# Optimization experiments

Hardware: AMD Instinct MI355X
Metric: run time of the kernel (lower is better)

## Reference

```python
import jax, jax.numpy as jnp
import numpy as np

DIM = 2048
N_HEADS = 32
HEAD_DIM = DIM // N_HEADS
D_FF = 4 * DIM
EPS = 1e-5


def layernorm(x, g, b):
    mu = jnp.mean(x, axis=-1, keepdims=True)
    var = jnp.mean(jnp.square(x - mu), axis=-1, keepdims=True)
    return (x - mu) * jax.lax.rsqrt(var + EPS) * g + b


def setup_inputs() -> dict:
    key = jax.random.key(0)
    ks = jax.random.split(key, 12)
    s = 0.02
    # Linear weights stored as [in, out] (y = x @ W + b), equivalent math to torch's x @ W.T
    return {
        "x": jax.random.normal(ks[0], (2, 2048, DIM), jnp.float32),
        "w_qkv": jax.random.normal(ks[1], (DIM, 3 * DIM), jnp.float32) * s,
        "b_qkv": jnp.zeros((3 * DIM,), jnp.float32),
        "w_o": jax.random.normal(ks[2], (DIM, DIM), jnp.float32) * s,
        "b_o": jnp.zeros((DIM,), jnp.float32),
        "g1": jnp.ones((DIM,), jnp.float32),
        "beta1": jnp.zeros((DIM,), jnp.float32),
        "w1": jax.random.normal(ks[3], (DIM, D_FF), jnp.float32) * s,
        "b1": jnp.zeros((D_FF,), jnp.float32),
        "w2": jax.random.normal(ks[4], (D_FF, DIM), jnp.float32) * s,
        "b2": jnp.zeros((DIM,), jnp.float32),
        "g2": jnp.ones((DIM,), jnp.float32),
        "beta2": jnp.zeros((DIM,), jnp.float32),
    }


def reference(x, w_qkv, b_qkv, w_o, b_o, g1, beta1, w1, b1, w2, b2, g2, beta2):
    B, T, _ = x.shape
    residual = x
    h = layernorm(x, g1, beta1)
    qkv = h @ w_qkv + b_qkv                      # [B,T,3*DIM]
    qkv = qkv.reshape(B, T, 3, N_HEADS, HEAD_DIM)
    qkv = jnp.transpose(qkv, (2, 0, 3, 1, 4))    # [3,B,H,T,D]
    q, k, v = qkv[0], qkv[1], qkv[2]
    scores = jnp.einsum("bhtd,bhsd->bhts", q, k) / np.sqrt(HEAD_DIM).astype(np.float32)
    attn = jax.nn.softmax(scores, axis=-1)       # full T x T (non-causal), as in source
    out = jnp.einsum("bhts,bhsd->bhtd", attn, v)
    out = jnp.transpose(out, (0, 2, 1, 3)).reshape(B, T, DIM)
    h = out @ w_o + b_o
    x = h + residual
    residual = x
    h = layernorm(x, g2, beta2)
    h = jax.nn.gelu(h @ w1 + b1, approximate=False)  # torch nn.GELU default = exact erf
    h = h @ w2 + b2
    return h + residual
```

## Files before the change

### kernel.cpp

```cpp
#include <hip/hip_runtime.h>
#include <hip/hip_bf16.h>

#define DIM  2048
#define DFF  8192
#define NH   32
#define HD   64
#define TT   2048
#define MM   4096

typedef __attribute__((ext_vector_type(4))) float f32x4;
typedef __attribute__((ext_vector_type(4))) unsigned int u32x4;
typedef __attribute__((ext_vector_type(2))) unsigned int u32x2;

#define MFMA16(ACC, A, B) \
  asm volatile("v_mfma_f32_16x16x32_bf16 %0, %1, %2, %0" : "+v"(ACC) : "v"(A), "v"(B))

#define GL16(GP, LP)                                                     \
  __builtin_amdgcn_global_load_lds(                                      \
      (const __attribute__((address_space(1))) void*)(GP),               \
      (__attribute__((address_space(3))) void*)(LP), 16, 0, 0)

__device__ __forceinline__ unsigned int f2bu(float f) {
  union { __hip_bfloat16 h; unsigned short u; } c;
  c.h = __float2bfloat16(f);
  return (unsigned int)c.u;
}

__global__ __launch_bounds__(256)
void transpose_cvt(const float* __restrict__ in, __hip_bfloat16* __restrict__ out,
                   int R, int C) {
  __shared__ float tile[32][33];
  const int tx = threadIdx.x, ty = threadIdx.y;
  const int bx = blockIdx.x * 32, by = blockIdx.y * 32;
#pragma unroll
  for (int i = 0; i < 32; i += 8)
    tile[ty + i][tx] = in[(size_t)(by + ty + i) * C + bx + tx];
  __syncthreads();
#pragma unroll
  for (int i = 0; i < 32; i += 8)
    out[(size_t)(bx + ty + i) * R + by + tx] = __float2bfloat16(tile[tx][ty + i]);
}

__global__ __launch_bounds__(256)
void ln_kernel(const float* __restrict__ in, const float* __restrict__ gw,
               const float* __restrict__ bw, __hip_bfloat16* __restrict__ out) {
  const int row = blockIdx.x;
  const int t = threadIdx.x;
  const float* x = in + (size_t)row * DIM;
  const float4 v0 = ((const float4*)x)[t * 2];
  const float4 v1 = ((const float4*)x)[t * 2 + 1];
  float s  = v0.x + v0.y + v0.z + v0.w + v1.x + v1.y + v1.z + v1.w;
  float ss = v0.x*v0.x + v0.y*v0.y + v0.z*v0.z + v0.w*v0.w
           + v1.x*v1.x + v1.y*v1.y + v1.z*v1.z + v1.w*v1.w;
#pragma unroll
  for (int o = 32; o >= 1; o >>= 1) { s += __shfl_xor(s, o); ss += __shfl_xor(ss, o); }
  __shared__ float red[8];
  if ((t & 63) == 0) { red[t >> 6] = s; red[4 + (t >> 6)] = ss; }
  __syncthreads();
  s  = red[0] + red[1] + red[2] + red[3];
  ss = red[4] + red[5] + red[6] + red[7];
  const float mean = s * (1.0f / DIM);
  const float rstd = rsqrtf(ss * (1.0f / DIM) - mean * mean + 1e-5f);
  const float4 g0 = ((const float4*)gw)[t * 2], g1 = ((const float4*)gw)[t * 2 + 1];
  const float4 b0 = ((const float4*)bw)[t * 2], b1 = ((const float4*)bw)[t * 2 + 1];
  uint4 o;
  o.x = f2bu((v0.x - mean) * rstd * g0.x + b0.x) | (f2bu((v0.y - mean) * rstd * g0.y + b0.y) << 16);
  o.y = f2bu((v0.z - mean) * rstd * g0.z + b0.z) | (f2bu((v0.w - mean) * rstd * g0.w + b0.w) << 16);
  o.z = f2bu((v1.x - mean) * rstd * g1.x + b1.x) | (f2bu((v1.y - mean) * rstd * g1.y + b1.y) << 16);
  o.w = f2bu((v1.z - mean) * rstd * g1.z + b1.z) | (f2bu((v1.w - mean) * rstd * g1.w + b1.w) << 16);
  *(uint4*)((char*)out + ((size_t)row * DIM + t * 8) * 2) = o;
}

template <int EPI>
__global__ __launch_bounds__(256)
void gemm_bt(const __hip_bfloat16* __restrict__ A, const __hip_bfloat16* __restrict__ Bt,
             const float* __restrict__ bias, const float* __restrict__ res,
             void* __restrict__ o0, void* __restrict__ o1, void* __restrict__ o2,
             int M, int N, int K) {
  __shared__ __hip_bfloat16 As[128 * 32];
  __shared__ __hip_bfloat16 Bs[128 * 32];
  const int tid = threadIdx.x;
  const int l = tid & 63, w = tid >> 6;
  const int wr = w >> 1, wc = w & 1;
  const int g = l >> 4, q15 = l & 15;
  const int bm = blockIdx.y * 128, bn = blockIdx.x * 128;

  f32x4 acc[4][4];
#pragma unroll
  for (int a = 0; a < 4; ++a)
#pragma unroll
    for (int b = 0; b < 4; ++b) acc[a][b] = (f32x4)0.0f;

  const __hip_bfloat16* aSrc = A  + (size_t)(bm + (tid >> 2)) * K + (tid & 3) * 8;
  const __hip_bfloat16* bSrc = Bt + (size_t)(bn + (tid >> 2)) * K + (tid & 3) * 8;
  __hip_bfloat16* aDst = As + tid * 8;
  __hip_bfloat16* bDst = Bs + tid * 8;
  const size_t rowStep = (size_t)64 * K;

  for (int kt = 0; kt < K; kt += 32) {
    GL16(aSrc + kt,            aDst);
    GL16(aSrc + rowStep + kt,  aDst + 2048);
    GL16(bSrc + kt,            bDst);
    GL16(bSrc + rowStep + kt,  bDst + 2048);
    __syncthreads();
    u32x4 af[4], bf[4];
#pragma unroll
    for (int rb = 0; rb < 4; ++rb)
      af[rb] = *(const u32x4*)(As + (wr * 64 + rb * 16 + q15) * 32 + g * 8);
#pragma unroll
    for (int cb = 0; cb < 4; ++cb)
      bf[cb] = *(const u32x4*)(Bs + (wc * 64 + cb * 16 + q15) * 32 + g * 8);
#pragma unroll
    for (int rb = 0; rb < 4; ++rb)
#pragma unroll
      for (int cb = 0; cb < 4; ++cb) MFMA16(acc[rb][cb], af[rb], bf[cb]);
    __syncthreads();
  }

#pragma unroll
  for (int rb = 0; rb < 4; ++rb) {
    const int row0 = bm + wr * 64 + rb * 16 + g * 4;
#pragma unroll
    for (int cb = 0; cb < 4; ++cb) {
      const int col = bn + wc * 64 + cb * 16 + q15;
      const float bv = bias[col];
#pragma unroll
      for (int i = 0; i < 4; ++i) {
        const int m = row0 + i;
        float v = acc[rb][cb][i] + bv;
        if constexpr (EPI == 0) {
          const int sel = col >> 11, hd = col & 2047, h = hd >> 6, d = hd & 63;
          const int b = m >> 11, t = m & 2047;
          if (sel == 0) {
            ((__hip_bfloat16*)o0)[((size_t)(b * NH + h) * TT + t) * HD + d] =
                __float2bfloat16(v * 0.125f);
          } else if (sel == 1) {
            ((__hip_bfloat16*)o1)[((size_t)(b * NH + h) * TT + t) * HD + d] =
                __float2bfloat16(v);
          } else {
            ((__hip_bfloat16*)o2)[((size_t)(b * NH + h) * HD + d) * TT + t] =
                __float2bfloat16(v);
          }
        } else if constexpr (EPI == 1) {
          ((float*)o0)[(size_t)m * N + col] = v + res[(size_t)m * N + col];
        } else if constexpr (EPI == 2) {
          ((__hip_bfloat16*)o0)[(size_t)m * N + col] =
              __float2bfloat16(0.5f * v * (1.0f + erff(v * 0.70710678118654752f)));
        } else {
          ((float*)o0)[(size_t)m * N + col] = v + res[(size_t)m * N + col];
        }
      }
    }
  }
}

__global__ __launch_bounds__(256)
void attn_kernel(const __hip_bfloat16* __restrict__ Q, const __hip_bfloat16* __restrict__ Kx,
                 const __hip_bfloat16* __restrict__ Vt, __hip_bfloat16* __restrict__ out) {
  __shared__ unsigned int Plds[4][2048];
  const int tid = threadIdx.x;
  const int l = tid & 63, w = tid >> 6;
  const int g = l >> 4, q15 = l & 15;
  const int bh = blockIdx.x >> 3;
  const int q0 = (blockIdx.x & 7) * 256 + w * 64;
  const __hip_bfloat16* Qb = Q  + (size_t)bh * TT * HD;
  const __hip_bfloat16* Kb = Kx + (size_t)bh * TT * HD;
  const __hip_bfloat16* Vb = Vt + (size_t)bh * HD * TT;
  unsigned int* Pw = Plds[w];

  u32x4 qf[4][2];
#pragma unroll
  for (int rb = 0; rb < 4; ++rb)
#pragma unroll
    for (int ks = 0; ks < 2; ++ks)
      qf[rb][ks] = *(const u32x4*)(Qb + (size_t)(q0 + rb * 16 + q15) * HD + ks * 32 + g * 8);

  f32x4 acc[4][4];
#pragma unroll
  for (int a = 0; a < 4; ++a)
#pragma unroll
    for (int b = 0; b < 4; ++b) acc[a][b] = (f32x4)0.0f;
  float mstat[4] = {-3e38f, -3e38f, -3e38f, -3e38f};
  float lstat[4] = {0.f, 0.f, 0.f, 0.f};

  for (int s0 = 0; s0 < TT; s0 += 64) {
    f32x4 st[4][4];
#pragma unroll
    for (int a = 0; a < 4; ++a)
#pragma unroll
      for (int b = 0; b < 4; ++b) st[a][b] = (f32x4)0.0f;
#pragma unroll
    for (int ks = 0; ks < 2; ++ks) {
      u32x4 kf[4];
#pragma unroll
      for (int cb = 0; cb < 4; ++cb)
        kf[cb] = *(const u32x4*)(Kb + (size_t)(s0 + cb * 16 + q15) * HD + ks * 32 + g * 8);
#pragma unroll
      for (int cb = 0; cb < 4; ++cb)
#pragma unroll
        for (int rb = 0; rb < 4; ++rb) MFMA16(st[cb][rb], kf[cb], qf[rb][ks]);
    }
#pragma unroll
    for (int rb = 0; rb < 4; ++rb) {
      float pm = st[0][rb][0];
#pragma unroll
      for (int cb = 0; cb < 4; ++cb)
#pragma unroll
        for (int i = 0; i < 4; ++i) pm = fmaxf(pm, st[cb][rb][i]);
      pm = fmaxf(pm, __shfl_xor(pm, 16));
      pm = fmaxf(pm, __shfl_xor(pm, 32));
      const float mnew = fmaxf(mstat[rb], pm);
      const float corr = __expf(mstat[rb] - mnew);
      mstat[rb] = mnew;
      float rs = 0.f;
#pragma unroll
      for (int cb = 0; cb < 4; ++cb)
#pragma unroll
        for (int i = 0; i < 4; ++i) {
          const float p = __expf(st[cb][rb][i] - mnew);
          st[cb][rb][i] = p;
          rs += p;
        }
      rs += __shfl_xor(rs, 16);
      rs += __shfl_xor(rs, 32);
      lstat[rb] = lstat[rb] * corr + rs;
#pragma unroll
      for (int db = 0; db < 4; ++db)
#pragma unroll
        for (int i = 0; i < 4; ++i) acc[db][rb][i] *= corr;
      const int row = rb * 16 + q15;
      const int rx = row & 7;
#pragma unroll
      for (int cb = 0; cb < 4; ++cb) {
        const unsigned int lo = f2bu(st[cb][rb][0]) | (f2bu(st[cb][rb][1]) << 16);
        const unsigned int hi = f2bu(st[cb][rb][2]) | (f2bu(st[cb][rb][3]) << 16);
        const int seg = (cb * 2 + (g >> 1)) ^ rx;
        u32x2 pk = {lo, hi};
        *(u32x2*)(Pw + row * 32 + seg * 4 + (g & 1) * 2) = pk;
      }
    }
#pragma unroll
    for (int ks2 = 0; ks2 < 2; ++ks2) {
      u32x4 vf[4], pf[4];
#pragma unroll
      for (int db = 0; db < 4; ++db)
        vf[db] = *(const u32x4*)(Vb + (size_t)(db * 16 + q15) * TT + s0 + ks2 * 32 + g * 8);
#pragma unroll
      for (int rb = 0; rb < 4; ++rb) {
        const int row = rb * 16 + q15;
        const int seg = (ks2 * 4 + g) ^ (row & 7);
        pf[rb] = *(const u32x4*)(Pw + row * 32 + seg * 4);
      }
#pragma unroll
      for (int db = 0; db < 4; ++db)
#pragma unroll
        for (int rb = 0; rb < 4; ++rb) MFMA16(acc[db][rb], vf[db], pf[rb]);
    }
  }
  const int b = bh >> 5, hh = bh & 31;
#pragma unroll
  for (int rb = 0; rb < 4; ++rb) {
    const float inv = 1.0f / lstat[rb];
    const size_t trow = (size_t)(b * TT + q0 + rb * 16 + q15);
#pragma unroll
    for (int db = 0; db < 4; ++db) {
      const unsigned int lo = f2bu(acc[db][rb][0] * inv) | (f2bu(acc[db][rb][1] * inv) << 16);
      const unsigned int hi = f2bu(acc[db][rb][2] * inv) | (f2bu(acc[db][rb][3] * inv) << 16);
      u32x2 pk = {lo, hi};
      *(u32x2*)(out + trow * DIM + hh * 64 + db * 16 + g * 4) = pk;
    }
  }
}

extern "C" void kernel_launch(void* const* d_in, const int* in_sizes, int n_in,
                              void* d_out, int out_size, void* d_ws, size_t ws_size,
                              hipStream_t stream) {
  (void)in_sizes; (void)n_in; (void)out_size; (void)ws_size;
  const float* x     = (const float*)d_in[0];
  const float* w_qkv = (const float*)d_in[1];
  const float* b_qkv = (const float*)d_in[2];
  const float* w_o   = (const float*)d_in[3];
  const float* b_o   = (const float*)d_in[4];
  const float* g1    = (const float*)d_in[5];
  const float* be1   = (const float*)d_in[6];
  const float* w1    = (const float*)d_in[7];
  const float* b1    = (const float*)d_in[8];
  const float* w2    = (const float*)d_in[9];
  const float* b2    = (const float*)d_in[10];
  const float* g2    = (const float*)d_in[11];
  const float* be2   = (const float*)d_in[12];

  char* ws = (char*)d_ws;
  size_t off = 0;
  auto alloc = [&](size_t bytes) {
    void* p = ws + off;
    off += (bytes + 255) & ~(size_t)255;
    return p;
  };
  __hip_bfloat16* WqkvT = (__hip_bfloat16*)alloc((size_t)6144 * 2048 * 2);
  __hip_bfloat16* WoT   = (__hip_bfloat16*)alloc((size_t)2048 * 2048 * 2);
  __hip_bfloat16* W1T   = (__hip_bfloat16*)alloc((size_t)8192 * 2048 * 2);
  __hip_bfloat16* W2T   = (__hip_bfloat16*)alloc((size_t)2048 * 8192 * 2);
  __hip_bfloat16* hbuf  = (__hip_bfloat16*)alloc((size_t)MM * DIM * 2);
  float*          xres  = (float*)alloc((size_t)MM * DIM * 4);
  __hip_bfloat16* Qb    = (__hip_bfloat16*)alloc((size_t)MM * DIM * 2);
  __hip_bfloat16* Kb    = (__hip_bfloat16*)alloc((size_t)MM * DIM * 2);
  __hip_bfloat16* Vtb   = (__hip_bfloat16*)alloc((size_t)MM * DIM * 2);
  __hip_bfloat16* attno = (__hip_bfloat16*)alloc((size_t)MM * DIM * 2);
  __hip_bfloat16* f1    = Qb;

  const dim3 tb(32, 8);
  transpose_cvt<<<dim3(6144 / 32, 2048 / 32), tb, 0, stream>>>(w_qkv, WqkvT, 2048, 6144);
  transpose_cvt<<<dim3(2048 / 32, 2048 / 32), tb, 0, stream>>>(w_o, WoT, 2048, 2048);
  transpose_cvt<<<dim3(8192 / 32, 2048 / 32), tb, 0, stream>>>(w1, W1T, 2048, 8192);
  transpose_cvt<<<dim3(2048 / 32, 8192 / 32), tb, 0, stream>>>(w2, W2T, 8192, 2048);

  ln_kernel<<<MM, 256, 0, stream>>>(x, g1, be1, hbuf);
  gemm_bt<0><<<dim3(6144 / 128, MM / 128), 256, 0, stream>>>(
      hbuf, WqkvT, b_qkv, nullptr, Qb, Kb, Vtb, MM, 6144, 2048);
  attn_kernel<<<512, 256, 0, stream>>>(Qb, Kb, Vtb, attno);
  gemm_bt<1><<<dim3(2048 / 128, MM / 128), 256, 0, stream>>>(
      attno, WoT, b_o, x, xres, nullptr, nullptr, MM, 2048, 2048);
  ln_kernel<<<MM, 256, 0, stream>>>(xres, g2, be2, hbuf);
  gemm_bt<2><<<dim3(8192 / 128, MM / 128), 256, 0, stream>>>(
      hbuf, W1T, b1, nullptr, f1, nullptr, nullptr, MM, 8192, 2048);
  gemm_bt<3><<<dim3(2048 / 128, MM / 128), 256, 0, stream>>>(
      f1, W2T, b2, xres, d_out, nullptr, nullptr, MM, 2048, 8192);
}
```

Baseline: 802.1 us.

## Remap GEMM tiles per XCD and streamline attention softmax with exp2 and lazy rescale

GEMM blocks use a 1D grid remapped so consecutive tiles go to the same XCD, which should improve L2 reuse of A and B panels. Q is pre-scaled by log2(e)/8 so the softmax can use the native v_exp_f32. The running-max rescale is skipped unless the new max exceeds the old one by more than 8. The attention loop also prefetches the next K tile into registers, uses max3 and packed bf16 conversion, and raises wave priority around the MFMA blocks. Skipping the rescale lets un-normalised values grow up to 2^8, which adds some numerical risk.

Measured after the change: 845.1 us. 5.4% more time.

```diff
diff --git a/kernel.cpp b/kernel.cpp
--- a/kernel.cpp
+++ b/kernel.cpp
@@ -11,6 +11,7 @@
 typedef __attribute__((ext_vector_type(4))) float f32x4;
 typedef __attribute__((ext_vector_type(4))) unsigned int u32x4;
 typedef __attribute__((ext_vector_type(2))) unsigned int u32x2;
+typedef unsigned short ushort_t;
 
 #define MFMA16(ACC, A, B) \
   asm volatile("v_mfma_f32_16x16x32_bf16 %0, %1, %2, %0" : "+v"(ACC) : "v"(A), "v"(B))
@@ -24,6 +25,17 @@
   union { __hip_bfloat16 h; unsigned short u; } c;
   c.h = __float2bfloat16(f);
   return (unsigned int)c.u;
+}
+__device__ __forceinline__ float fexp2(float x) {
+  float r; asm("v_exp_f32 %0, %1" : "=v"(r) : "v"(x)); return r;
+}
+__device__ __forceinline__ unsigned cvtpk(float lo, float hi) {
+  unsigned r; asm("v_cvt_pk_bf16_f32 %0, %1, %2" : "=v"(r) : "v"(lo), "v"(hi));
+  return r;
+}
+__device__ __forceinline__ float fmax3(float a, float b, float c) {
+  float r; asm("v_max3_f32 %0, %1, %2, %3" : "=v"(r) : "v"(a), "v"(b), "v"(c));
+  return r;
 }
 
 __global__ __launch_bounds__(256)
@@ -83,7 +95,16 @@
   const int l = tid & 63, w = tid >> 6;
   const int wr = w >> 1, wc = w & 1;
   const int g = l >> 4, q15 = l & 15;
-  const int bm = blockIdx.y * 128, bn = blockIdx.x * 128;
+
+  const int nby = M >> 7;
+  const int nwg = (N >> 7) * nby;
+  int id = blockIdx.x;
+  {
+    const int cpx = nwg >> 3;
+    id = (id & 7) * cpx + (id >> 3);
+  }
+  const int bm = (id % nby) << 7;
+  const int bn = (id / nby) << 7;
 
   f32x4 acc[4][4];
 #pragma unroll
@@ -133,7 +154,7 @@
           const int b = m >> 11, t = m & 2047;
           if (sel == 0) {
             ((__hip_bfloat16*)o0)[((size_t)(b * NH + h) * TT + t) * HD + d] =
-                __float2bfloat16(v * 0.125f);
+                __float2bfloat16(v * 0.18033688011112042f);
           } else if (sel == 1) {
             ((__hip_bfloat16*)o1)[((size_t)(b * NH + h) * TT + t) * HD + d] =
                 __float2bfloat16(v);
@@ -183,79 +204,96 @@
   float mstat[4] = {-3e38f, -3e38f, -3e38f, -3e38f};
   float lstat[4] = {0.f, 0.f, 0.f, 0.f};
 
+  u32x4 kf[2][4];
+#pragma unroll
+  for (int cb = 0; cb < 4; ++cb)
+#pragma unroll
+    for (int ks = 0; ks < 2; ++ks)
+      kf[ks][cb] = *(const u32x4*)(Kb + (size_t)(cb * 16 + q15) * HD + ks * 32 + g * 8);
+
   for (int s0 = 0; s0 < TT; s0 += 64) {
     f32x4 st[4][4];
 #pragma unroll
     for (int a = 0; a < 4; ++a)
 #pragma unroll
       for (int b = 0; b < 4; ++b) st[a][b] = (f32x4)0.0f;
-#pragma unroll
-    for (int ks = 0; ks < 2; ++ks) {
-      u32x4 kf[4];
+    __builtin_amdgcn_s_setprio(1);
+#pragma unroll
+    for (int ks = 0; ks < 2; ++ks)
 #pragma unroll
       for (int cb = 0; cb < 4; ++cb)
-        kf[cb] = *(const u32x4*)(Kb + (size_t)(s0 + cb * 16 + q15) * HD + ks * 32 + g * 8);
+#pragma unroll
+        for (int rb = 0; rb < 4; ++rb) MFMA16(st[cb][rb], kf[ks][cb], qf[rb][ks]);
+    __builtin_amdgcn_s_setprio(0);
+    if (s0 + 64 < TT) {
 #pragma unroll
       for (int cb = 0; cb < 4; ++cb)
 #pragma unroll
-        for (int rb = 0; rb < 4; ++rb) MFMA16(st[cb][rb], kf[cb], qf[rb][ks]);
+        for (int ks = 0; ks < 2; ++ks)
+          kf[ks][cb] = *(const u32x4*)(Kb + (size_t)(s0 + 64 + cb * 16 + q15) * HD + ks * 32 + g * 8);
     }
 #pragma unroll
     for (int rb = 0; rb < 4; ++rb) {
-      float pm = st[0][rb][0];
-#pragma unroll
-      for (int cb = 0; cb < 4; ++cb)
-#pragma unroll
-        for (int i = 0; i < 4; ++i) pm = fmaxf(pm, st[cb][rb][i]);
+      float a0 = fmax3(st[0][rb][0], st[0][rb][1], st[0][rb][2]);
+      float a1 = fmax3(st[0][rb][3], st[1][rb][0], st[1][rb][1]);
+      float a2 = fmax3(st[1][rb][2], st[1][rb][3], st[2][rb][0]);
+      float a3 = fmax3(st[2][rb][1], st[2][rb][2], st[2][rb][3]);
+      float a4 = fmax3(st[3][rb][0], st[3][rb][1], st[3][rb][2]);
+      float pm = fmax3(fmax3(a0, a1, a2), a3, fmax3(a4, st[3][rb][3], a0));
       pm = fmaxf(pm, __shfl_xor(pm, 16));
       pm = fmaxf(pm, __shfl_xor(pm, 32));
-      const float mnew = fmaxf(mstat[rb], pm);
-      const float corr = __expf(mstat[rb] - mnew);
-      mstat[rb] = mnew;
+      if (!__all(pm <= mstat[rb] + 8.0f)) {
+        const float mnew = fmaxf(mstat[rb], pm);
+        const float corr = fexp2(mstat[rb] - mnew);
+        mstat[rb] = mnew;
+        lstat[rb] *= corr;
+#pragma unroll
+        for (int db = 0; db < 4; ++db)
+#pragma unroll
+          for (int i = 0; i < 4; ++i) acc[db][rb][i] *= corr;
+      }
+      const float mcur = mstat[rb];
       float rs = 0.f;
-#pragma unroll
-      for (int cb = 0; cb < 4; ++cb)
-#pragma unroll
-        for (int i = 0; i < 4; ++i) {
-          const float p = __expf(st[cb][rb][i] - mnew);
-          st[cb][rb][i] = p;
-          rs += p;
-        }
+      const int row = rb * 16 + q15;
+      const int rx = row & 7;
+#pragma unroll
+      for (int cb = 0; cb < 4; ++cb) {
+        const float p0 = fexp2(st[cb][rb][0] - mcur);
+        const float p1 = fexp2(st[cb][rb][1] - mcur);
+        const float p2 = fexp2(st[cb][rb][2] - mcur);
+        const float p3 = fexp2(st[cb][rb][3] - mcur);
+        rs += (p0 + p1) + (p2 + p3);
+        const int seg = (cb * 2 + (g >> 1)) ^ rx;
+        u32x2 pk = {cvtpk(p0, p1), cvtpk(p2, p3)};
+        *(u32x2*)(Pw + row * 32 + seg * 4 + (g & 1) * 2) = pk;
+      }
       rs += __shfl_xor(rs, 16);
       rs += __shfl_xor(rs, 32);
-      lstat[rb] = lstat[rb] * corr + rs;
+      lstat[rb] += rs;
+    }
+    u32x4 vf[2][4];
+#pragma unroll
+    for (int ks2 = 0; ks2 < 2; ++ks2)
 #pragma unroll
       for (int db = 0; db < 4; ++db)
-#pragma unroll
-        for (int i = 0; i < 4; ++i) acc[db][rb][i] *= corr;
-      const int row = rb * 16 + q15;
-      const int rx = row & 7;
-#pragma unroll
-      for (int cb = 0; cb < 4; ++cb) {
-        const unsigned int lo = f2bu(st[cb][rb][0]) | (f2bu(st[cb][rb][1]) << 16);
-        const unsigned int hi = f2bu(st[cb][rb][2]) | (f2bu(st[cb][rb][3]) << 16);
-        const int seg = (cb * 2 + (g >> 1)) ^ rx;
-        u32x2 pk = {lo, hi};
-        *(u32x2*)(Pw + row * 32 + seg * 4 + (g & 1) * 2) = pk;
-      }
-    }
-#pragma unroll
-    for (int ks2 = 0; ks2 < 2; ++ks2) {
-      u32x4 vf[4], pf[4];
-#pragma unroll
-      for (int db = 0; db < 4; ++db)
-        vf[db] = *(const u32x4*)(Vb + (size_t)(db * 16 + q15) * TT + s0 + ks2 * 32 + g * 8);
+        vf[ks2][db] = *(const u32x4*)(Vb + (size_t)(db * 16 + q15) * TT + s0 + ks2 * 32 + g * 8);
+    u32x4 pf[2][4];
+#pragma unroll
+    for (int ks2 = 0; ks2 < 2; ++ks2)
 #pragma unroll
       for (int rb = 0; rb < 4; ++rb) {
         const int row = rb * 16 + q15;
         const int seg = (ks2 * 4 + g) ^ (row & 7);
-        pf[rb] = *(const u32x4*)(Pw + row * 32 + seg * 4);
+        pf[ks2][rb] = *(const u32x4*)(Pw + row * 32 + seg * 4);
       }
+    __builtin_amdgcn_s_setprio(1);
+#pragma unroll
+    for (int ks2 = 0; ks2 < 2; ++ks2)
 #pragma unroll
       for (int db = 0; db < 4; ++db)
 #pragma unroll
-        for (int rb = 0; rb < 4; ++rb) MFMA16(acc[db][rb], vf[db], pf[rb]);
-    }
+        for (int rb = 0; rb < 4; ++rb) MFMA16(acc[db][rb], vf[ks2][db], pf[ks2][rb]);
+    __builtin_amdgcn_s_setprio(0);
   }
   const int b = bh >> 5, hh = bh & 31;
 #pragma unroll
@@ -264,9 +302,8 @@
     const size_t trow = (size_t)(b * TT + q0 + rb * 16 + q15);
 #pragma unroll
     for (int db = 0; db < 4; ++db) {
-      const unsigned int lo = f2bu(acc[db][rb][0] * inv) | (f2bu(acc[db][rb][1] * inv) << 16);
-      const unsigned int hi = f2bu(acc[db][rb][2] * inv) | (f2bu(acc[db][rb][3] * inv) << 16);
-      u32x2 pk = {lo, hi};
+      u32x2 pk = {cvtpk(acc[db][rb][0] * inv, acc[db][rb][1] * inv),
+                  cvtpk(acc[db][rb][2] * inv, acc[db][rb][3] * inv)};
       *(u32x2*)(out + trow * DIM + hh * 64 + db * 16 + g * 4) = pk;
     }
   }
@@ -316,14 +353,14 @@
   transpose_cvt<<<dim3(2048 / 32, 8192 / 32), tb, 0, stream>>>(w2, W2T, 8192, 2048);
 
   ln_kernel<<<MM, 256, 0, stream>>>(x, g1, be1, hbuf);
-  gemm_bt<0><<<dim3(6144 / 128, MM / 128), 256, 0, stream>>>(
+  gemm_bt<0><<<(MM / 128) * (6144 / 128), 256, 0, stream>>>(
       hbuf, WqkvT, b_qkv, nullptr, Qb, Kb, Vtb, MM, 6144, 2048);
   attn_kernel<<<512, 256, 0, stream>>>(Qb, Kb, Vtb, attno);
-  gemm_bt<1><<<dim3(2048 / 128, MM / 128), 256, 0, stream>>>(
+  gemm_bt<1><<<(MM / 128) * (2048 / 128), 256, 0, stream>>>(
       attno, WoT, b_o, x, xres, nullptr, nullptr, MM, 2048, 2048);
   ln_kernel<<<MM, 256, 0, stream>>>(xres, g2, be2, hbuf);
-  gemm_bt<2><<<dim3(8192 / 128, MM / 128), 256, 0, stream>>>(
+  gemm_bt<2><<<(MM / 128) * (8192 / 128), 256, 0, stream>>>(
       hbuf, W1T, b1, nullptr, f1, nullptr, nullptr, MM, 8192, 2048);
-  gemm_bt<3><<<dim3(2048 / 128, MM / 128), 256, 0, stream>>>(
+  gemm_bt<3><<<(MM / 128) * (2048 / 128), 256, 0, stream>>>(
       f1, W2T, b2, xres, d_out, nullptr, nullptr, MM, 2048, 8192);
 }
```
